# Performance work log

Hardware: AMD Instinct MI355X
Metric: run time of the kernel (lower is better)

The kernel has to match this reference:

```python
import jax, jax.numpy as jnp
import numpy as np
from jax import lax

BN_EPS = 1e-5


def _spatial_gate(x, w, g, b, m, v):
    # x: [N, C, H, W]; ChannelPool -> [N, 2, H, W]; 7x7 conv -> [N,1,H,W]; BN (eval); sigmoid gate
    comp = jnp.stack([jnp.max(x, axis=1), jnp.mean(x, axis=1)], axis=1)
    o = lax.conv_general_dilated(comp, w, (1, 1), [(3, 3), (3, 3)],
                                 dimension_numbers=('NCHW', 'OIHW', 'NCHW'))
    o = (o - m[None, :, None, None]) * lax.rsqrt(v + BN_EPS)[None, :, None, None] \
        * g[None, :, None, None] + b[None, :, None, None]
    s = jax.nn.sigmoid(o)
    return x * s


def _eca_sort(x, w_eca):
    # global avg pool -> sort channels desc -> 1D conv over sorted seq -> sigmoid -> unsort -> gate
    y = jnp.mean(x, axis=(2, 3))               # [N, C]
    order = jnp.argsort(-y, axis=1)            # descending sort indices
    rank = jnp.argsort(order, axis=1)          # inverse permutation
    ys = jnp.take_along_axis(y, order, axis=1)  # sorted descending
    k = w_eca.shape[-1]
    p = k // 2
    o = lax.conv_general_dilated(ys[:, None, :], w_eca, (1,), [(p, p)],
                                 dimension_numbers=('NCH', 'OIH', 'NCH'))[:, 0, :]
    sig = jax.nn.sigmoid(o)
    yr = jnp.take_along_axis(sig, rank, axis=1)  # reorder back per original index_select(rank)
    return x * yr[:, :, None, None]


def setup_inputs() -> dict:
    key = jax.random.key(0)
    ks = jax.random.split(key, 6)
    N, C, H, W = 32, 256, 56, 56
    inp = {
        'x': jax.random.normal(ks[0], (N, C, H, W), dtype=jnp.float32),
        'weight': jax.random.normal(ks[1], (1,), dtype=jnp.float32),
        'w_h': jax.random.normal(ks[2], (1, 2, 7, 7), dtype=jnp.float32) * 0.1,
        'g_h': jnp.ones((1,), jnp.float32), 'b_h': jnp.zeros((1,), jnp.float32),
        'm_h': jnp.zeros((1,), jnp.float32), 'v_h': jnp.ones((1,), jnp.float32),
        'w_w': jax.random.normal(ks[3], (1, 2, 7, 7), dtype=jnp.float32) * 0.1,
        'g_w': jnp.ones((1,), jnp.float32), 'b_w': jnp.zeros((1,), jnp.float32),
        'm_w': jnp.zeros((1,), jnp.float32), 'v_w': jnp.ones((1,), jnp.float32),
        'w_s': jax.random.normal(ks[4], (1, 2, 7, 7), dtype=jnp.float32) * 0.1,
        'g_s': jnp.ones((1,), jnp.float32), 'b_s': jnp.zeros((1,), jnp.float32),
        'm_s': jnp.zeros((1,), jnp.float32), 'v_s': jnp.ones((1,), jnp.float32),
        'w_eca': jax.random.normal(ks[5], (1, 1, 5), dtype=jnp.float32) * 0.3,
    }
    return inp


def reference(x, weight, w_h, g_h, b_h, m_h, v_h, w_w, g_w, b_w, m_w, v_w,
              w_s, g_s, b_s, m_s, v_s, w_eca):
    # branch 1: gate over H-as-channel (permute 0,2,1,3)
    xh = jnp.transpose(x, (0, 2, 1, 3))
    x11 = jnp.transpose(_spatial_gate(xh, w_h, g_h, b_h, m_h, v_h), (0, 2, 1, 3))
    # branch 2: gate over W-as-channel (permute 0,3,2,1)
    xw = jnp.transpose(x, (0, 3, 2, 1))
    x21 = jnp.transpose(_spatial_gate(xw, w_w, g_w, b_w, m_w, v_w), (0, 3, 2, 1))
    # branch 3: eca with sort/unsort
    x31 = _eca_sort(x, w_eca)
    # branch 4: plain spatial gate
    xo = _spatial_gate(x, w_s, g_s, b_s, m_s, v_s)
    return 0.23779 * xo + 0.24695 * x11 + 0.24365 * x21 + 0.27173 * x31
```

## Files before the change

kernel.cpp:

```cpp
#include <hip/hip_runtime.h>
#include <math.h>

#define N_ 32
#define C_ 256
#define H_ 56
#define W_ 56
#define HW_ (H_*W_)
#define CHW_ (C_*HW_)
#define NHW_ (N_*HW_)
#define NCW_ (N_*C_*W_)
#define NHC_ (N_*H_*C_)
#define BN_EPS_ 1e-5f

#define NB_CP (NHW_ / 4 / 64)
#define TLD 60

__global__ __launch_bounds__(64) void pools_k(
        const float* __restrict__ x,
        float* __restrict__ maxC, float* __restrict__ meanC,
        float* __restrict__ maxH, float* __restrict__ meanH,
        float* __restrict__ maxW, float* __restrict__ meanW,
        float* __restrict__ y) {
    int b = blockIdx.x;
    int lane = threadIdx.x;
    const float4* x4 = (const float4*)x;
    if (b < NB_CP) {
        int t = b * 64 + lane;
        int n = t / (HW_ / 4);
        int hw4 = t - n * (HW_ / 4);
        size_t base = (size_t)n * (CHW_ / 4) + hw4;
        float4 mx = make_float4(-INFINITY, -INFINITY, -INFINITY, -INFINITY);
        float4 sm = make_float4(0.f, 0.f, 0.f, 0.f);
        #pragma unroll 8
        for (int c = 0; c < C_; ++c) {
            float4 v = x4[base + (size_t)c * (HW_ / 4)];
            mx.x = fmaxf(mx.x, v.x); mx.y = fmaxf(mx.y, v.y);
            mx.z = fmaxf(mx.z, v.z); mx.w = fmaxf(mx.w, v.w);
            sm.x += v.x; sm.y += v.y; sm.z += v.z; sm.w += v.w;
        }
        sm.x *= (1.f / C_); sm.y *= (1.f / C_); sm.z *= (1.f / C_); sm.w *= (1.f / C_);
        ((float4*)maxC)[t] = mx;
        ((float4*)meanC)[t] = sm;
    } else {
        __shared__ float tile[28 * TLD];
        int pb = b - NB_CP;
        int n = pb >> 8, c = pb & 255;
        size_t pbase = (size_t)pb * (HW_ / 4);
        float cmx = -INFINITY, csm = 0.f;
        #pragma unroll
        for (int s = 0; s < 2; ++s) {
            #pragma unroll
            for (int i = 0; i < 6; ++i) {
                int j = i * 64 + lane;
                float4 v = x4[pbase + s * 392 + j];
                int hl = j / 14, w4 = j - hl * 14;
                float* d = &tile[hl * TLD + w4 * 4];
                d[0] = v.x; d[1] = v.y; d[2] = v.z; d[3] = v.w;
            }
            if (lane < 8) {
                int j = 384 + lane;
                float4 v = x4[pbase + s * 392 + j];
                int hl = j / 14, w4 = j - hl * 14;
                float* d = &tile[hl * TLD + w4 * 4];
                d[0] = v.x; d[1] = v.y; d[2] = v.z; d[3] = v.w;
            }
            __syncthreads();
            if (lane < W_) {
                #pragma unroll 7
                for (int hl = 0; hl < 28; ++hl) {
                    float v = tile[hl * TLD + lane];
                    cmx = fmaxf(cmx, v); csm += v;
                }
            }
            if (lane < 28) {
                int h = s * 28 + lane;
                const float4* r = (const float4*)&tile[lane * TLD];
                float4 m4 = make_float4(-INFINITY, -INFINITY, -INFINITY, -INFINITY);
                float4 s4 = make_float4(0.f, 0.f, 0.f, 0.f);
                #pragma unroll
                for (int k = 0; k < 14; ++k) {
                    float4 v = r[k];
                    m4.x = fmaxf(m4.x, v.x); m4.y = fmaxf(m4.y, v.y);
                    m4.z = fmaxf(m4.z, v.z); m4.w = fmaxf(m4.w, v.w);
                    s4.x += v.x; s4.y += v.y; s4.z += v.z; s4.w += v.w;
                }
                int o = (n * H_ + h) * C_ + c;
                maxW[o] = fmaxf(fmaxf(m4.x, m4.y), fmaxf(m4.z, m4.w));
                meanW[o] = (s4.x + s4.y + s4.z + s4.w) * (1.f / W_);
            }
            __syncthreads();
        }
        if (lane < W_) {
            int o = (n * C_ + c) * W_ + lane;
            maxH[o] = cmx;
            meanH[o] = csm * (1.f / H_);
        }
        float tot = csm;
        #pragma unroll
        for (int m = 32; m >= 1; m >>= 1) tot += __shfl_xor(tot, m);
        if (lane == 0) y[n * C_ + c] = tot * (1.f / HW_);
    }
}

__device__ __forceinline__ void conv7_part(int t, const float* __restrict__ p0,
                                           const float* __restrict__ p1,
                                           const float* __restrict__ wt,
                                           float g, float bb, float m, float v,
                                           float* __restrict__ out, int R, int Cc) {
    int per = R * Cc;
    int n = t / per;
    int r2 = t - n * per;
    int i = r2 / Cc, j = r2 - i * Cc;
    const float* b0 = p0 + (size_t)n * per;
    const float* b1 = p1 + (size_t)n * per;
    float acc = 0.f;
    #pragma unroll
    for (int ki = 0; ki < 7; ++ki) {
        int ii = i + ki - 3;
        if (ii < 0 || ii >= R) continue;
        #pragma unroll
        for (int kj = 0; kj < 7; ++kj) {
            int jj = j + kj - 3;
            if (jj < 0 || jj >= Cc) continue;
            int idx = ii * Cc + jj;
            acc += b0[idx] * wt[ki * 7 + kj] + b1[idx] * wt[49 + ki * 7 + kj];
        }
    }
    float o = (acc - m) * rsqrtf(v + BN_EPS_) * g + bb;
    out[t] = 1.f / (1.f + expf(-o));
}

#define NB_SS (NHW_ / 256)
#define NB_SH (NCW_ / 256)
#define NB_SW (NHC_ / 256)

__global__ __launch_bounds__(256) void conv_eca_k(
        const float* __restrict__ maxC, const float* __restrict__ meanC,
        const float* __restrict__ maxH, const float* __restrict__ meanH,
        const float* __restrict__ maxW, const float* __restrict__ meanW,
        const float* __restrict__ w_s, const float* __restrict__ g_s,
        const float* __restrict__ b_s, const float* __restrict__ m_s,
        const float* __restrict__ v_s,
        const float* __restrict__ w_h, const float* __restrict__ g_h,
        const float* __restrict__ b_h, const float* __restrict__ m_h,
        const float* __restrict__ v_h,
        const float* __restrict__ w_w, const float* __restrict__ g_w,
        const float* __restrict__ b_w, const float* __restrict__ m_w,
        const float* __restrict__ v_w,
        const float* __restrict__ y, const float* __restrict__ w_eca,
        float* __restrict__ s_s, float* __restrict__ s_h, float* __restrict__ s_w,
        float* __restrict__ gate) {
    __shared__ float sv[C_];
    __shared__ int si[C_];
    int b = blockIdx.x;
    int tid = threadIdx.x;
    if (b < NB_SS) {
        conv7_part(b * 256 + tid, maxC, meanC, w_s, g_s[0], b_s[0], m_s[0], v_s[0],
                   s_s, H_, W_);
    } else if (b < NB_SS + NB_SH) {
        conv7_part((b - NB_SS) * 256 + tid, maxH, meanH, w_h, g_h[0], b_h[0], m_h[0],
                   v_h[0], s_h, C_, W_);
    } else if (b < NB_SS + NB_SH + NB_SW) {
        conv7_part((b - NB_SS - NB_SH) * 256 + tid, maxW, meanW, w_w, g_w[0], b_w[0],
                   m_w[0], v_w[0], s_w, H_, C_);
    } else {
        int n = b - (NB_SS + NB_SH + NB_SW);
        sv[tid] = y[n * C_ + tid];
        si[tid] = tid;
        __syncthreads();
        for (int k = 2; k <= C_; k <<= 1) {
            for (int j = k >> 1; j > 0; j >>= 1) {
                int ixj = tid ^ j;
                if (ixj > tid) {
                    float v1 = sv[tid], v2 = sv[ixj];
                    int i1 = si[tid], i2 = si[ixj];
                    bool before = (v1 > v2) || (v1 == v2 && i1 < i2);
                    bool dir = ((tid & k) == 0);
                    if (dir ? !before : before) {
                        sv[tid] = v2; sv[ixj] = v1;
                        si[tid] = i2; si[ixj] = i1;
                    }
                }
                __syncthreads();
            }
        }
        float o = 0.f;
        #pragma unroll
        for (int j = 0; j < 5; ++j) {
            int p = tid + j - 2;
            if (p >= 0 && p < C_) o += sv[p] * w_eca[j];
        }
        gate[n * C_ + si[tid]] = 1.f / (1.f + expf(-o));
    }
}

__global__ __launch_bounds__(256) void apply_k(
        const float* __restrict__ x, const float* __restrict__ s_s,
        const float* __restrict__ s_h, const float* __restrict__ s_w,
        const float* __restrict__ gate, float* __restrict__ out) {
    int t = blockIdx.x * 256 + threadIdx.x;
    int f = t * 4;
    int n = f / CHW_;
    int rem = f - n * CHW_;
    int c = rem / HW_;
    int hw = rem - c * HW_;
    int h = hw / W_;
    int w = hw - h * W_;
    float4 xv = ((const float4*)x)[t];
    float4 s4 = *(const float4*)(s_s + (size_t)n * HW_ + hw);
    float4 h4 = *(const float4*)(s_h + ((size_t)n * C_ + c) * W_ + w);
    float sw = s_w[((size_t)n * H_ + h) * C_ + c];
    float ge = gate[n * C_ + c];
    float base = 0.24365f * sw + 0.27173f * ge;
    float4 o;
    o.x = xv.x * (0.23779f * s4.x + 0.24695f * h4.x + base);
    o.y = xv.y * (0.23779f * s4.y + 0.24695f * h4.y + base);
    o.z = xv.z * (0.23779f * s4.z + 0.24695f * h4.z + base);
    o.w = xv.w * (0.23779f * s4.w + 0.24695f * h4.w + base);
    ((float4*)out)[t] = o;
}

extern "C" void kernel_launch(void* const* d_in, const int* in_sizes, int n_in,
                              void* d_out, int out_size, void* d_ws, size_t ws_size,
                              hipStream_t stream) {
    const float* x     = (const float*)d_in[0];
    const float* w_h   = (const float*)d_in[2];
    const float* g_h   = (const float*)d_in[3];
    const float* b_h   = (const float*)d_in[4];
    const float* m_h   = (const float*)d_in[5];
    const float* v_h   = (const float*)d_in[6];
    const float* w_w   = (const float*)d_in[7];
    const float* g_w   = (const float*)d_in[8];
    const float* b_w   = (const float*)d_in[9];
    const float* m_w   = (const float*)d_in[10];
    const float* v_w   = (const float*)d_in[11];
    const float* w_s   = (const float*)d_in[12];
    const float* g_s   = (const float*)d_in[13];
    const float* b_s   = (const float*)d_in[14];
    const float* m_s   = (const float*)d_in[15];
    const float* v_s   = (const float*)d_in[16];
    const float* w_eca = (const float*)d_in[17];
    float* out = (float*)d_out;

    float* ws    = (float*)d_ws;
    float* maxC  = ws;
    float* meanC = maxC  + NHW_;
    float* maxH  = meanC + NHW_;
    float* meanH = maxH  + NCW_;
    float* maxW  = meanH + NCW_;
    float* meanW = maxW  + NHC_;
    float* s_s   = meanW + NHC_;
    float* s_h   = s_s   + NHW_;
    float* s_w   = s_h   + NCW_;
    float* yv    = s_w   + NHC_;
    float* gate  = yv    + N_ * C_;

    pools_k<<<NB_CP + N_ * C_, 64, 0, stream>>>(x, maxC, meanC, maxH, meanH,
                                                maxW, meanW, yv);

    int conv_blocks = NB_SS + NB_SH + NB_SW + N_;
    conv_eca_k<<<conv_blocks, 256, 0, stream>>>(maxC, meanC, maxH, meanH, maxW, meanW,
                                                w_s, g_s, b_s, m_s, v_s,
                                                w_h, g_h, b_h, m_h, v_h,
                                                w_w, g_w, b_w, m_w, v_w,
                                                yv, w_eca, s_s, s_h, s_w, gate);

    apply_k<<<(N_ * CHW_ / 4) / 256, 256, 0, stream>>>(x, s_s, s_h, s_w, gate, out);
}
```

Measured before the change: 108.6 us.

## Pack pool planes into 256-thread blocks and split channel-pool across waves

The pooling kernel now uses 256-thread blocks, each of the four waves handling one (n,c) plane for the H/W pools. The channel max/mean reduction is split so each wave reduces 64 channels and a shared-memory step combines the partial results. This aims to raise parallelism and shorten the serial 256-channel loop in the channel-pool blocks. The conv helper is also templated on its dimensions so divisions become compile-time constants. The larger shared-memory footprint per block could limit occupancy.

```diff
diff --git a/kernel.cpp b/kernel.cpp
--- a/kernel.cpp
+++ b/kernel.cpp
@@ -12,38 +12,24 @@
 #define NHC_ (N_*H_*C_)
 #define BN_EPS_ 1e-5f
 
-#define NB_CP (NHW_ / 4 / 64)
 #define TLD 60
-
-__global__ __launch_bounds__(64) void pools_k(
+#define NB_PL 2048
+#define NB_CP 392
+
+__global__ __launch_bounds__(256) void pools_k(
         const float* __restrict__ x,
         float* __restrict__ maxC, float* __restrict__ meanC,
         float* __restrict__ maxH, float* __restrict__ meanH,
         float* __restrict__ maxW, float* __restrict__ meanW,
         float* __restrict__ y) {
+    __shared__ float smem[4 * 28 * TLD];
     int b = blockIdx.x;
-    int lane = threadIdx.x;
+    int tid = threadIdx.x;
+    int wave = tid >> 6, lane = tid & 63;
     const float4* x4 = (const float4*)x;
-    if (b < NB_CP) {
-        int t = b * 64 + lane;
-        int n = t / (HW_ / 4);
-        int hw4 = t - n * (HW_ / 4);
-        size_t base = (size_t)n * (CHW_ / 4) + hw4;
-        float4 mx = make_float4(-INFINITY, -INFINITY, -INFINITY, -INFINITY);
-        float4 sm = make_float4(0.f, 0.f, 0.f, 0.f);
-        #pragma unroll 8
-        for (int c = 0; c < C_; ++c) {
-            float4 v = x4[base + (size_t)c * (HW_ / 4)];
-            mx.x = fmaxf(mx.x, v.x); mx.y = fmaxf(mx.y, v.y);
-            mx.z = fmaxf(mx.z, v.z); mx.w = fmaxf(mx.w, v.w);
-            sm.x += v.x; sm.y += v.y; sm.z += v.z; sm.w += v.w;
-        }
-        sm.x *= (1.f / C_); sm.y *= (1.f / C_); sm.z *= (1.f / C_); sm.w *= (1.f / C_);
-        ((float4*)maxC)[t] = mx;
-        ((float4*)meanC)[t] = sm;
-    } else {
-        __shared__ float tile[28 * TLD];
-        int pb = b - NB_CP;
+    if (b < NB_PL) {
+        float* tile = &smem[wave * 28 * TLD];
+        int pb = b * 4 + wave;
         int n = pb >> 8, c = pb & 255;
         size_t pbase = (size_t)pb * (HW_ / 4);
         float cmx = -INFINITY, csm = 0.f;
@@ -99,15 +85,56 @@
         #pragma unroll
         for (int m = 32; m >= 1; m >>= 1) tot += __shfl_xor(tot, m);
         if (lane == 0) y[n * C_ + c] = tot * (1.f / HW_);
+    } else {
+        float4* smx = (float4*)smem;
+        float4* ssm = smx + 256;
+        int bb = b - NB_PL;
+        int q = bb * 64 + lane;
+        int n = q / (HW_ / 4);
+        int hw4 = q - n * (HW_ / 4);
+        size_t base = (size_t)n * (CHW_ / 4) + hw4 + (size_t)(wave * 64) * (HW_ / 4);
+        float4 mx = make_float4(-INFINITY, -INFINITY, -INFINITY, -INFINITY);
+        float4 sm = make_float4(0.f, 0.f, 0.f, 0.f);
+        #pragma unroll 8
+        for (int i = 0; i < 64; ++i) {
+            float4 v = x4[base + (size_t)i * (HW_ / 4)];
+            mx.x = fmaxf(mx.x, v.x); mx.y = fmaxf(mx.y, v.y);
+            mx.z = fmaxf(mx.z, v.z); mx.w = fmaxf(mx.w, v.w);
+            sm.x += v.x; sm.y += v.y; sm.z += v.z; sm.w += v.w;
+        }
+        smx[wave * 64 + lane] = mx;
+        ssm[wave * 64 + lane] = sm;
+        __syncthreads();
+        if (tid < 64) {
+            float4 m = smx[tid];
+            #pragma unroll
+            for (int j = 1; j < 4; ++j) {
+                float4 v = smx[j * 64 + tid];
+                m.x = fmaxf(m.x, v.x); m.y = fmaxf(m.y, v.y);
+                m.z = fmaxf(m.z, v.z); m.w = fmaxf(m.w, v.w);
+            }
+            ((float4*)maxC)[bb * 64 + tid] = m;
+        } else if (tid < 128) {
+            int t2 = tid - 64;
+            float4 s = ssm[t2];
+            #pragma unroll
+            for (int j = 1; j < 4; ++j) {
+                float4 v = ssm[j * 64 + t2];
+                s.x += v.x; s.y += v.y; s.z += v.z; s.w += v.w;
+            }
+            s.x *= (1.f / C_); s.y *= (1.f / C_); s.z *= (1.f / C_); s.w *= (1.f / C_);
+            ((float4*)meanC)[bb * 64 + t2] = s;
+        }
     }
 }
 
+template <int R, int Cc>
 __device__ __forceinline__ void conv7_part(int t, const float* __restrict__ p0,
                                            const float* __restrict__ p1,
                                            const float* __restrict__ wt,
                                            float g, float bb, float m, float v,
-                                           float* __restrict__ out, int R, int Cc) {
-    int per = R * Cc;
+                                           float* __restrict__ out) {
+    const int per = R * Cc;
     int n = t / per;
     int r2 = t - n * per;
     int i = r2 / Cc, j = r2 - i * Cc;
@@ -155,14 +182,14 @@
     int b = blockIdx.x;
     int tid = threadIdx.x;
     if (b < NB_SS) {
-        conv7_part(b * 256 + tid, maxC, meanC, w_s, g_s[0], b_s[0], m_s[0], v_s[0],
-                   s_s, H_, W_);
+        conv7_part<H_, W_>(b * 256 + tid, maxC, meanC, w_s, g_s[0], b_s[0], m_s[0],
+                           v_s[0], s_s);
     } else if (b < NB_SS + NB_SH) {
-        conv7_part((b - NB_SS) * 256 + tid, maxH, meanH, w_h, g_h[0], b_h[0], m_h[0],
-                   v_h[0], s_h, C_, W_);
+        conv7_part<C_, W_>((b - NB_SS) * 256 + tid, maxH, meanH, w_h, g_h[0], b_h[0],
+                           m_h[0], v_h[0], s_h);
     } else if (b < NB_SS + NB_SH + NB_SW) {
-        conv7_part((b - NB_SS - NB_SH) * 256 + tid, maxW, meanW, w_w, g_w[0], b_w[0],
-                   m_w[0], v_w[0], s_w, H_, C_);
+        conv7_part<H_, C_>((b - NB_SS - NB_SH) * 256 + tid, maxW, meanW, w_w, g_w[0],
+                           b_w[0], m_w[0], v_w[0], s_w);
     } else {
         int n = b - (NB_SS + NB_SH + NB_SW);
         sv[tid] = y[n * C_ + tid];
@@ -255,8 +282,8 @@
     float* yv    = s_w   + NHC_;
     float* gate  = yv    + N_ * C_;
 
-    pools_k<<<NB_CP + N_ * C_, 64, 0, stream>>>(x, maxC, meanC, maxH, meanH,
-                                                maxW, meanW, yv);
+    pools_k<<<NB_PL + NB_CP, 256, 0, stream>>>(x, maxC, meanC, maxH, meanH,
+                                               maxW, meanW, yv);
 
     int conv_blocks = NB_SS + NB_SH + NB_SW + N_;
     conv_eca_k<<<conv_blocks, 256, 0, stream>>>(maxC, meanC, maxH, meanH, maxW, meanW,
```

New measurement: 103.4 us. 1.05x faster.
